# Kernel optimization log

Measured on AMD Instinct MI355X. Metric: run time of the kernel, lower is better.

The kernel has to match this reference:

```python
import jax, jax.numpy as jnp
import numpy as np

SIZES = [11793, 2948, 737, 184]   # vertices per mesh level, fine -> coarse
SPIRAL = [20, 14, 12, 9]          # spiral length per level
FILT = [128, 128, 64, 3]          # filters_dec[0]
LATENT = 128
BATCH = 16


def setup_inputs() -> dict:
    key = jax.random.key(0)
    ks = jax.random.split(key, 12)
    V = [s + 1 for s in SIZES]  # +1 dummy vertex per level
    inp = {}
    inp["z"] = jax.random.normal(ks[0], (BATCH, LATENT), jnp.float32)
    # dense upsampling matrices: level k+1 -> level k
    inp["U0"] = jax.random.normal(ks[1], (V[0], V[1]), jnp.float32) * 0.02
    inp["U1"] = jax.random.normal(ks[2], (V[1], V[2]), jnp.float32) * 0.02
    inp["U2"] = jax.random.normal(ks[3], (V[2], V[3]), jnp.float32) * 0.02
    # spiral index tables per level (shared across batch, values in [0, V))
    inp["S0"] = jax.random.randint(ks[4], (V[0], SPIRAL[0]), 0, V[0], dtype=jnp.int32)
    inp["S1"] = jax.random.randint(ks[5], (V[1], SPIRAL[1]), 0, V[1], dtype=jnp.int32)
    inp["S2"] = jax.random.randint(ks[6], (V[2], SPIRAL[2]), 0, V[2], dtype=jnp.int32)
    # fc_latent_dec: latent -> (sizes[-1]+1)*filters_dec[0][0]
    inp["Wfc"] = jax.random.normal(ks[7], (LATENT, V[3] * FILT[0]), jnp.float32) * 0.02
    inp["bfc"] = jnp.zeros((V[3] * FILT[0],), jnp.float32)
    # SpiralConv linear weights, stored (K*F_in, F_out), K-major flatten as in torch
    inp["W0"] = jax.random.normal(ks[8], (SPIRAL[2] * FILT[0], FILT[1]), jnp.float32) * 0.02
    inp["b0"] = jnp.zeros((FILT[1],), jnp.float32)
    inp["W1"] = jax.random.normal(ks[9], (SPIRAL[1] * FILT[1], FILT[2]), jnp.float32) * 0.02
    inp["b1"] = jnp.zeros((FILT[2],), jnp.float32)
    inp["W2"] = jax.random.normal(ks[10], (SPIRAL[0] * FILT[2], FILT[3]), jnp.float32) * 0.02
    inp["b2"] = jnp.zeros((FILT[3],), jnp.float32)
    return inp


def spiral_conv(x, S, W, b, elu):
    # x: (B, V, F); S: (V, K) vertex indices into the same level
    B, V, F = x.shape
    K = S.shape[1]
    g = jnp.take(x, S.reshape(-1), axis=1).reshape(B, V, K * F)  # gather, K-major flatten
    out = g @ W + b  # (B, V, F_out)
    if elu:
        out = jax.nn.elu(out)
    # zero out the dummy (last) vertex, as in Neural3DMM's zero_padding mask
    return out.at[:, -1, :].set(0.0)


def reference(z, U0, U1, U2, S0, S1, S2, Wfc, bfc, W0, b0, W1, b1, W2, b2):
    B = z.shape[0]
    x = (z @ Wfc + bfc).reshape(B, SIZES[-1] + 1, FILT[0])  # (B, 185, 128)
    x = jnp.einsum('vw,bwf->bvf', U2, x)                    # upsample -> (B, 738, 128)
    x = spiral_conv(x, S2, W0, b0, True)                    # (B, 738, 128)
    x = jnp.einsum('vw,bwf->bvf', U1, x)                    # (B, 2949, 128)
    x = spiral_conv(x, S1, W1, b1, True)                    # (B, 2949, 64)
    x = jnp.einsum('vw,bwf->bvf', U0, x)                    # (B, 11794, 64)
    x = spiral_conv(x, S0, W2, b2, False)                   # identity act -> (B, 11794, 3)
    return x
```

## Files before the change

### kernel.cpp

```cpp
#include <hip/hip_runtime.h>
#include <cmath>


#define NB 16

typedef __attribute__((ext_vector_type(8))) short bf16x8;
typedef __attribute__((ext_vector_type(4))) float f32x4;

__device__ __forceinline__ unsigned short f2bf(float x) {
    union { float f; unsigned u; } v; v.f = x;
    unsigned r = v.u + 0x7FFFu + ((v.u >> 16) & 1u);
    return (unsigned short)(r >> 16);
}
__device__ __forceinline__ void gload16(const void* src, void* dst) {
    __builtin_amdgcn_global_load_lds(
        (const __attribute__((address_space(1))) unsigned int*)src,
        (__attribute__((address_space(3))) unsigned int*)dst, 16, 0, 0);
}

__global__ __launch_bounds__(256) void cvt_u_all(
    const float* __restrict__ U0, const float* __restrict__ U1,
    const float* __restrict__ U2, unsigned short* __restrict__ Ub0,
    unsigned short* __restrict__ Ub1, unsigned short* __restrict__ Ub2) {
    int k = blockIdx.x * 256 + threadIdx.x;
    int r = blockIdx.y;
    const float* src;
    unsigned short* dst;
    int V, W, Wp, row;
    if (r < 11904) {
        src = U0; dst = Ub0; V = 11794; W = 2949; Wp = 2976; row = r;
    } else if (r < 11904 + 3072) {
        src = U1; dst = Ub1; V = 2949; W = 738; Wp = 768; row = r - 11904;
    } else {
        src = U2; dst = Ub2; V = 738; W = 185; Wp = 192; row = r - 11904 - 3072;
    }
    if (k >= Wp) return;
    float v = (row < V && k < W) ? src[(size_t)row * W + k] : 0.f;
    dst[(size_t)row * Wp + k] = f2bf(v);
}

__global__ __launch_bounds__(256) void cvt_misc(
    const float* __restrict__ W0, const float* __restrict__ W1,
    const float* __restrict__ W2, const int* __restrict__ S0,
    const int* __restrict__ S1, const int* __restrict__ S2,
    unsigned short* __restrict__ W0T, unsigned short* __restrict__ W1T,
    unsigned short* __restrict__ W2T, int* __restrict__ S0T,
    int* __restrict__ S1T, int* __restrict__ S2T) {
    const int N0 = 128 * 1536, N1 = 64 * 1792, N2 = 16 * 1288;
    const int N3 = 20 * 11794, N4 = 14 * 2949, N5 = 12 * 738;
    int id = blockIdx.x * 256 + threadIdx.x;
    if (id < N0) {
        int n = id / 1536, k = id - n * 1536;
        W0T[id] = f2bf(W0[(size_t)k * 128 + n]);
        return;
    }
    id -= N0;
    if (id < N1) {
        int n = id / 1792, k = id - n * 1792;
        W1T[id] = f2bf(W1[(size_t)k * 64 + n]);
        return;
    }
    id -= N1;
    if (id < N2) {
        int n = id / 1288, k = id - n * 1288;
        float v = (n < 3 && k < 1280) ? W2[(size_t)k * 3 + n] : 0.f;
        W2T[id] = f2bf(v);
        return;
    }
    id -= N2;
    if (id < N3) {
        int k = id / 11794, v = id - k * 11794;
        S0T[id] = S0[(size_t)v * 20 + k];
        return;
    }
    id -= N3;
    if (id < N4) {
        int k = id / 2949, v = id - k * 2949;
        S1T[id] = S1[(size_t)v * 14 + k];
        return;
    }
    id -= N4;
    if (id < N5) {
        int k = id / 738, v = id - k * 738;
        S2T[id] = S2[(size_t)v * 12 + k];
    }
}

__global__ __launch_bounds__(256) void fc_kernel(const float* __restrict__ z,
                                                 const float* __restrict__ Wfc,
                                                 const float* __restrict__ bfc,
                                                 unsigned short* __restrict__ x3T) {
    const int N = 185 * 128;
    __shared__ float zs[NB * 128];
    int t = threadIdx.x;
    for (int i = t; i < NB * 128; i += 256) zs[i] = z[i];
    __syncthreads();
    int n = blockIdx.x * 256 + t;
    if (n >= N) return;
    float acc[NB];
#pragma unroll
    for (int b = 0; b < NB; ++b) acc[b] = 0.f;
    for (int k = 0; k < 128; ++k) {
        float w = Wfc[k * N + n];
#pragma unroll
        for (int b = 0; b < NB; ++b) acc[b] = fmaf(zs[b * 128 + k], w, acc[b]);
    }
    float bv = bfc[n];
    int f = n & 127, v = n >> 7;
#pragma unroll
    for (int b = 0; b < NB; ++b)
        x3T[(size_t)(b * 128 + f) * 192 + v] = f2bf(acc[b] + bv);
    if (n < 7 * 128) {
        int vp = 185 + (n >> 7);
#pragma unroll
        for (int b = 0; b < NB; ++b)
            x3T[(size_t)(b * 128 + f) * 192 + vp] = 0;
    }
}

template<int FSH, int VP>
__global__ __launch_bounds__(256) void ups_mfma(
    const unsigned short* __restrict__ Ub, const unsigned short* __restrict__ xT,
    unsigned short* __restrict__ out,
    int WpA, int WpB, int nsteps, int gxsh, int q) {
    const int F = 1 << FSH;
    __shared__ __align__(16) unsigned short As[3][128 * 32];
    __shared__ __align__(16) unsigned short Bs[3][128 * 32];
    const int t = threadIdx.x;
    const int wv = t >> 6, lane = t & 63;
    const int lr = lane & 15;

    const int flat = blockIdx.x;
    const int wg = (flat & 7) * q + (flat >> 3);
    const int m0 = (wg >> gxsh) * 128;
    const int n0 = (wg & ((1 << gxsh) - 1)) * 128;

    const int srow = lane >> 2;
    const int schunk = (((lane & 3) - ((lane >> 3) & 3)) & 3) * 8;
    const int ii0 = wv * 2, ii1 = wv * 2 + 1;
    const unsigned short* asrc0 = Ub + (size_t)(m0 + ii0 * 16 + srow) * WpA + schunk;
    const unsigned short* asrc1 = Ub + (size_t)(m0 + ii1 * 16 + srow) * WpA + schunk;
    const unsigned short* bsrc0 = xT + (size_t)(n0 + ii0 * 16 + srow) * WpB + schunk;
    const unsigned short* bsrc1 = xT + (size_t)(n0 + ii1 * 16 + srow) * WpB + schunk;

    const int fslot = (((lane >> 4) + (lr >> 1)) & 3) * 8;
    const int wrow = (wv >> 1) * 64;
    const int wcol = (wv & 1) * 64;
    const int u0 = wv * 1024;

    f32x4 acc[4][4];
#pragma unroll
    for (int i = 0; i < 4; ++i)
#pragma unroll
        for (int j = 0; j < 4; ++j) acc[i][j] = {0.f, 0.f, 0.f, 0.f};

#define UPS_STAGE(off_, B_)                                             \
    {                                                                   \
        gload16(asrc0 + (off_), &As[B_][u0]);                           \
        gload16(bsrc0 + (off_), &Bs[B_][u0]);                           \
        gload16(asrc1 + (off_), &As[B_][u0 + 512]);                     \
        gload16(bsrc1 + (off_), &Bs[B_][u0 + 512]);                     \
    }
#define UPS_COMPUTE(B_)                                                 \
    {                                                                   \
        bf16x8 af[4], bg[4];                                            \
        _Pragma("unroll")                                               \
        for (int mt = 0; mt < 4; ++mt)                                  \
            af[mt] = *(const bf16x8*)&As[B_][(wrow + mt * 16 + lr) * 32 + fslot]; \
        _Pragma("unroll")                                               \
        for (int nt = 0; nt < 4; ++nt)                                  \
            bg[nt] = *(const bf16x8*)&Bs[B_][(wcol + nt * 16 + lr) * 32 + fslot]; \
        _Pragma("unroll")                                               \
        for (int mt = 0; mt < 4; ++mt)                                  \
            _Pragma("unroll")                                           \
            for (int nt = 0; nt < 4; ++nt)                              \
                acc[mt][nt] = __builtin_amdgcn_mfma_f32_16x16x32_bf16(  \
                    af[mt], bg[nt], acc[mt][nt], 0, 0, 0);              \
    }
#define UPS_WAIT4 asm volatile("s_waitcnt vmcnt(4)" ::: "memory"); __builtin_amdgcn_s_barrier();
#define UPS_WAIT0 asm volatile("s_waitcnt vmcnt(0)" ::: "memory"); __builtin_amdgcn_s_barrier();

    UPS_STAGE(0, 0);
    UPS_STAGE(32, 1);
    UPS_WAIT4;

    const int m = nsteps / 3;
    for (int it = 0; it < m - 1; ++it) {
        UPS_STAGE(64, 2);  UPS_COMPUTE(0); UPS_WAIT4;
        UPS_STAGE(96, 0);  UPS_COMPUTE(1); UPS_WAIT4;
        UPS_STAGE(128, 1); UPS_COMPUTE(2); UPS_WAIT4;
        asrc0 += 96; asrc1 += 96; bsrc0 += 96; bsrc1 += 96;
    }
    UPS_STAGE(64, 2);
    UPS_COMPUTE(0); UPS_WAIT4;
    UPS_COMPUTE(1); UPS_WAIT0;
    UPS_COMPUTE(2);
#undef UPS_STAGE
#undef UPS_COMPUTE
#undef UPS_WAIT4
#undef UPS_WAIT0

#pragma unroll
    for (int mt = 0; mt < 4; ++mt) {
        const int vb = m0 + wrow + mt * 16 + (lane >> 4) * 4;
#pragma unroll
        for (int nt = 0; nt < 4; ++nt) {
            const int col = n0 + wcol + nt * 16 + lr;
            const int b = col >> FSH, f = col & (F - 1);
            unsigned short* op = out + (size_t)b * VP * F + f;
#pragma unroll
            for (int j = 0; j < 4; ++j)
                op[(size_t)(vb + j) * F] = f2bf(acc[mt][nt][j]);
        }
    }
}

template<int VP>
__global__ __launch_bounds__(64) void conv_mfma(
    const unsigned short* __restrict__ xu, const int* __restrict__ ST,
    const unsigned short* __restrict__ WT, const float* __restrict__ bias,
    unsigned short* __restrict__ outT,
    int VT, int Ksp, int Kdim, int nsteps, int Fout) {
    __shared__ __align__(16) unsigned short As[2][32 * 32];
    __shared__ __align__(16) unsigned short Bs[2][64 * 32];
    const int lane = threadIdx.x;
    const int lr = lane & 15;
    const int m0 = blockIdx.x * 32;
    const int n0 = blockIdx.y * 64;
    const int b = m0 / VP;
    const int v0 = m0 - b * VP;
    const unsigned short* xb = xu + (((size_t)b * VP) << 7);

    const int arow = lane >> 1;
    const int h = lane & 1;
    const int vg = (v0 + arow < VT) ? (v0 + arow) : (VT - 1);
    const int schunk = (((lane & 3) - ((lane >> 3) & 3)) & 3) * 8;
    const int fslot = (((lane >> 4) + (lr >> 1)) & 3) * 8;
    int sw0 = arow * 32 + (((2 * h + 0 + ((lane >> 2) & 3)) & 3) * 8);
    int sw1 = arow * 32 + (((2 * h + 1 + ((lane >> 2) & 3)) & 3) * 8);

    int s_c = 0;
    int idx_c = ST[vg];
    int idx_n = ST[(size_t)VT + vg];

    f32x4 acc[2][4];
#pragma unroll
    for (int i = 0; i < 2; ++i)
#pragma unroll
        for (int j = 0; j < 4; ++j) acc[i][j] = {0.f, 0.f, 0.f, 0.f};

#define CONV_COMPUTE(B_)                                                \
    {                                                                   \
        bf16x8 af[2], bg[4];                                            \
        _Pragma("unroll")                                               \
        for (int mt = 0; mt < 2; ++mt)                                  \
            af[mt] = *(const bf16x8*)&As[B_][(mt * 16 + lr) * 32 + fslot]; \
        _Pragma("unroll")                                               \
        for (int nt = 0; nt < 4; ++nt)                                  \
            bg[nt] = *(const bf16x8*)&Bs[B_][(nt * 16 + lr) * 32 + fslot]; \
        _Pragma("unroll")                                               \
        for (int mt = 0; mt < 2; ++mt)                                  \
            _Pragma("unroll")                                           \
            for (int nt = 0; nt < 4; ++nt)                              \
                acc[mt][nt] = __builtin_amdgcn_mfma_f32_16x16x32_bf16(  \
                    af[mt], bg[nt], acc[mt][nt], 0, 0, 0);              \
    }
#define CONV_BODY(tn_, CUR_, NXT_)                                      \
    {                                                                   \
        const int k0 = (tn_) * 32;                                      \
        const int sn = k0 >> 7;                                         \
        const int idx = (sn != s_c) ? idx_n : idx_c;                    \
        const unsigned short* p = xb + (((size_t)idx) << 7) + (k0 & 127) + h * 16; \
        bf16x8 g0 = *(const bf16x8*)(p);                                \
        bf16x8 g1 = *(const bf16x8*)(p + 8);                            \
        _Pragma("unroll")                                               \
        for (int i = 0; i < 4; ++i) {                                   \
            const int n = n0 + i * 16 + (lane >> 2);                    \
            gload16(WT + (size_t)n * Kdim + k0 + schunk, &Bs[NXT_][i * 512]); \
        }                                                               \
        if (sn != s_c) {                                                \
            idx_c = idx_n; s_c = sn;                                    \
            if (s_c + 1 < Ksp) idx_n = ST[(size_t)(s_c + 1) * VT + vg]; \
        }                                                               \
        CONV_COMPUTE(CUR_);                                             \
        *(bf16x8*)&As[NXT_][sw0] = g0;                                  \
        *(bf16x8*)&As[NXT_][sw1] = g1;                                  \
        __syncthreads();                                                \
    }

    {
        const unsigned short* p = xb + (((size_t)idx_c) << 7) + h * 16;
        bf16x8 g0 = *(const bf16x8*)(p);
        bf16x8 g1 = *(const bf16x8*)(p + 8);
#pragma unroll
        for (int i = 0; i < 4; ++i) {
            const int n = n0 + i * 16 + (lane >> 2);
            gload16(WT + (size_t)n * Kdim + schunk, &Bs[0][i * 512]);
        }
        *(bf16x8*)&As[0][sw0] = g0;
        *(bf16x8*)&As[0][sw1] = g1;
    }
    __syncthreads();

    for (int ts = 0; ts + 2 < nsteps; ts += 2) {
        CONV_BODY(ts + 1, 0, 1);
        CONV_BODY(ts + 2, 1, 0);
    }
    CONV_BODY(nsteps - 1, 0, 1);
    CONV_COMPUTE(1);
#undef CONV_BODY
#undef CONV_COMPUTE

#pragma unroll
    for (int nt = 0; nt < 4; ++nt) {
        const int n = n0 + nt * 16 + lr;
        const float bv = bias[n];
        unsigned short* op = outT + (size_t)(b * Fout + n) * VP;
#pragma unroll
        for (int mt = 0; mt < 2; ++mt) {
            const int v = v0 + mt * 16 + (lane >> 4) * 4;
            ushort4 stv;
#pragma unroll
            for (int j = 0; j < 4; ++j) {
                float val = acc[mt][nt][j] + bv;
                val = val > 0.f ? val : expm1f(val);
                if (v + j == VT - 1) val = 0.f;
                ((unsigned short*)&stv)[j] = f2bf(val);
            }
            *(ushort4*)(op + v) = stv;
        }
    }
}

__global__ __launch_bounds__(64) void out_mfma(
    const unsigned short* __restrict__ xu, const int* __restrict__ ST,
    const unsigned short* __restrict__ W2T, const float* __restrict__ b2,
    float* __restrict__ out) {
    const int VT = 11794, VP = 11904, TPB = 372;
    __shared__ __align__(16) unsigned short As[2][32 * 32];
    const int lane = threadIdx.x;
    const int lr = lane & 15;
    const int lko = (lane >> 4) * 8;
    const int bm = blockIdx.x;
    const int b = bm / TPB;
    const int v0 = (bm - b * TPB) * 32;
    const unsigned short* xb = xu + ((size_t)b * VP << 6);

    const int arow = lane >> 1;
    const int h = lane & 1;
    const int v = v0 + arow;
    const int vg = v < VT ? v : VT - 1;
    int sw0 = arow * 32 + (((2 * h + 0 + ((lane >> 2) & 3)) & 3) * 8);
    int sw1 = arow * 32 + (((2 * h + 1 + ((lane >> 2) & 3)) & 3) * 8);
    const int fslot = (((lane >> 4) + (lr >> 1)) & 3) * 8;

    int s_c = 0;
    int idx_c = ST[vg];
    int idx_n = ST[VT + vg];

    f32x4 acc[2];
    acc[0] = {0.f, 0.f, 0.f, 0.f};
    acc[1] = {0.f, 0.f, 0.f, 0.f};

    const unsigned short* wrow = W2T + (size_t)lr * 1288 + lko;
    bf16x8 bg_c = *(const bf16x8*)(wrow);

#define OUT_COMPUTE(B_)                                                 \
    {                                                                   \
        bf16x8 af[2];                                                   \
        _Pragma("unroll")                                               \
        for (int mt = 0; mt < 2; ++mt)                                  \
            af[mt] = *(const bf16x8*)&As[B_][(mt * 16 + lr) * 32 + fslot]; \
        _Pragma("unroll")                                               \
        for (int mt = 0; mt < 2; ++mt)                                  \
            acc[mt] = __builtin_amdgcn_mfma_f32_16x16x32_bf16(af[mt], bg_c, acc[mt], 0, 0, 0); \
    }
#define OUT_BODY(tn_, CUR_, NXT_)                                       \
    {                                                                   \
        const int k0 = (tn_) * 32;                                      \
        const int sn = k0 >> 6;                                         \
        const int idx = (sn != s_c) ? idx_n : idx_c;                    \
        const unsigned short* p = xb + (((size_t)idx) << 6) + (k0 & 63) + h * 16; \
        bf16x8 g0 = *(const bf16x8*)(p);                                \
        bf16x8 g1 = *(const bf16x8*)(p + 8);                            \
        bf16x8 bg_n = *(const bf16x8*)(wrow + k0);                      \
        if (sn != s_c) {                                                \
            idx_c = idx_n; s_c = sn;                                    \
            if (s_c + 1 < 20) idx_n = ST[(size_t)(s_c + 1) * VT + vg];  \
        }                                                               \
        OUT_COMPUTE(CUR_);                                              \
        bg_c = bg_n;                                                    \
        *(bf16x8*)&As[NXT_][sw0] = g0;                                  \
        *(bf16x8*)&As[NXT_][sw1] = g1;                                  \
        __syncthreads();                                                \
    }

    {
        const unsigned short* p = xb + ((size_t)idx_c << 6) + h * 16;
        bf16x8 g0 = *(const bf16x8*)(p);
        bf16x8 g1 = *(const bf16x8*)(p + 8);
        *(bf16x8*)&As[0][sw0] = g0;
        *(bf16x8*)&As[0][sw1] = g1;
    }
    __syncthreads();

    const int nsteps = 40;
    for (int ts = 0; ts + 2 < nsteps; ts += 2) {
        OUT_BODY(ts + 1, 0, 1);
        OUT_BODY(ts + 2, 1, 0);
    }
    OUT_BODY(nsteps - 1, 0, 1);
    OUT_COMPUTE(1);
#undef OUT_BODY
#undef OUT_COMPUTE

    if (lr < 3) {
        const float bv = b2[lr];
#pragma unroll
        for (int mt = 0; mt < 2; ++mt) {
#pragma unroll
            for (int j = 0; j < 4; ++j) {
                const int vv = v0 + mt * 16 + (lane >> 4) * 4 + j;
                if (vv < VT) {
                    float val = acc[mt][j] + bv;
                    if (vv == VT - 1) val = 0.f;
                    out[((size_t)b * VT + vv) * 3 + lr] = val;
                }
            }
        }
    }
}

extern "C" void kernel_launch(void* const* d_in, const int* in_sizes, int n_in,
                              void* d_out, int out_size, void* d_ws, size_t ws_size,
                              hipStream_t stream) {
    const float* z   = (const float*)d_in[0];
    const float* U0  = (const float*)d_in[1];
    const float* U1  = (const float*)d_in[2];
    const float* U2  = (const float*)d_in[3];
    const int*   S0  = (const int*)d_in[4];
    const int*   S1  = (const int*)d_in[5];
    const int*   S2  = (const int*)d_in[6];
    const float* Wfc = (const float*)d_in[7];
    const float* bfc = (const float*)d_in[8];
    const float* W0  = (const float*)d_in[9];
    const float* b0  = (const float*)d_in[10];
    const float* W1  = (const float*)d_in[11];
    const float* b1  = (const float*)d_in[12];
    const float* W2  = (const float*)d_in[13];
    const float* b2  = (const float*)d_in[14];
    float* out = (float*)d_out;

    char* ws = (char*)d_ws;
    unsigned short* Ub0 = (unsigned short*)(ws + 0);
    unsigned short* Ub1 = (unsigned short*)(ws + 70852608);
    unsigned short* Ub2 = (unsigned short*)(ws + 75571200);
    unsigned short* x3T = (unsigned short*)(ws + 75866112);
    unsigned short* x2u = (unsigned short*)(ws + 76652544);
    unsigned short* x2T = (unsigned short*)(ws + 79798272);
    unsigned short* x1u = (unsigned short*)(ws + 82944000);
    unsigned short* x1T = (unsigned short*)(ws + 95526912);
    unsigned short* x0u = (unsigned short*)(ws + 101818368);
    unsigned short* W0T = (unsigned short*)(ws + 126197760);
    unsigned short* W1T = (unsigned short*)(ws + 126590976);
    int* S1T = (int*)(ws + 126820352);
    int* S2T = (int*)(ws + 126985504);
    int* S0T = (int*)(ws + 127020928);
    unsigned short* W2T = (unsigned short*)(ws + 127964448);

    cvt_u_all<<<dim3(12, 11904 + 3072 + 768), 256, 0, stream>>>(U0, U1, U2, Ub0, Ub1, Ub2);
    {
        const int total = 128 * 1536 + 64 * 1792 + 16 * 1288 +
                          20 * 11794 + 14 * 2949 + 12 * 738;
        cvt_misc<<<dim3((total + 255) / 256), 256, 0, stream>>>(
            W0, W1, W2, S0, S1, S2, W0T, W1T, W2T, S0T, S1T, S2T);
    }

    fc_kernel<<<dim3((185 * 128 + 255) / 256), 256, 0, stream>>>(z, Wfc, bfc, x3T);
    ups_mfma<7, 768><<<dim3(96), 256, 0, stream>>>(Ub2, x3T, x2u, 192, 192, 6, 4, 12);
    conv_mfma<768><<<dim3(384, 2), 64, 0, stream>>>(x2u, S2T, W0T, b0, x2T, 738, 12, 1536, 48, 128);
    ups_mfma<7, 3072><<<dim3(384), 256, 0, stream>>>(Ub1, x2T, x1u, 768, 768, 24, 4, 48);
    conv_mfma<3072><<<dim3(1536, 1), 64, 0, stream>>>(x1u, S1T, W1T, b1, x1T, 2949, 14, 1792, 56, 64);
    ups_mfma<6, 11904><<<dim3(744), 256, 0, stream>>>(Ub0, x1T, x0u, 2976, 3072, 93, 3, 93);
    out_mfma<<<dim3(16 * 372), 64, 0, stream>>>(x0u, S0T, W2T, b2, out);
}
```

Measured before the change: 362.9 us.

## Fully unroll spiral conv loops, preload indices, drop barriers for waitcnt pipelining

conv_mfma now takes the step count and spiral length as template parameters. Both conv_mfma and out_mfma load every spiral index into registers up front and fully unroll the K loop. conv_mfma triple-buffers the weight tiles in LDS and replaces __syncthreads with explicit s_waitcnt vmcnt so more global loads stay in flight. out_mfma drops its barriers, relying on single-wave in-order LDS access. This removes per-step branch, index-fetch and barrier overhead, at the cost of more registers and reliance on correct manual wait counts.

```diff
diff --git a/kernel.cpp b/kernel.cpp
--- a/kernel.cpp
+++ b/kernel.cpp
@@ -215,14 +215,14 @@
     }
 }
 
-template<int VP>
+template<int VP, int NSTEPS, int KSP>
 __global__ __launch_bounds__(64) void conv_mfma(
     const unsigned short* __restrict__ xu, const int* __restrict__ ST,
     const unsigned short* __restrict__ WT, const float* __restrict__ bias,
     unsigned short* __restrict__ outT,
-    int VT, int Ksp, int Kdim, int nsteps, int Fout) {
+    int VT, int Kdim, int Fout) {
     __shared__ __align__(16) unsigned short As[2][32 * 32];
-    __shared__ __align__(16) unsigned short Bs[2][64 * 32];
+    __shared__ __align__(16) unsigned short Bs[3][64 * 32];
     const int lane = threadIdx.x;
     const int lr = lane & 15;
     const int m0 = blockIdx.x * 32;
@@ -236,12 +236,12 @@
     const int vg = (v0 + arow < VT) ? (v0 + arow) : (VT - 1);
     const int schunk = (((lane & 3) - ((lane >> 3) & 3)) & 3) * 8;
     const int fslot = (((lane >> 4) + (lr >> 1)) & 3) * 8;
-    int sw0 = arow * 32 + (((2 * h + 0 + ((lane >> 2) & 3)) & 3) * 8);
-    int sw1 = arow * 32 + (((2 * h + 1 + ((lane >> 2) & 3)) & 3) * 8);
-
-    int s_c = 0;
-    int idx_c = ST[vg];
-    int idx_n = ST[(size_t)VT + vg];
+    const int sw0 = arow * 32 + (((2 * h + 0 + ((lane >> 2) & 3)) & 3) * 8);
+    const int sw1 = arow * 32 + (((2 * h + 1 + ((lane >> 2) & 3)) & 3) * 8);
+
+    int idx[KSP];
+#pragma unroll
+    for (int k = 0; k < KSP; ++k) idx[k] = ST[(size_t)k * VT + vg];
 
     f32x4 acc[2][4];
 #pragma unroll
@@ -249,15 +249,17 @@
 #pragma unroll
         for (int j = 0; j < 4; ++j) acc[i][j] = {0.f, 0.f, 0.f, 0.f};
 
-#define CONV_COMPUTE(B_)                                                \
+    bf16x8 gA[2][2];
+
+#define CC(AB_, BB_)                                                    \
     {                                                                   \
         bf16x8 af[2], bg[4];                                            \
         _Pragma("unroll")                                               \
         for (int mt = 0; mt < 2; ++mt)                                  \
-            af[mt] = *(const bf16x8*)&As[B_][(mt * 16 + lr) * 32 + fslot]; \
+            af[mt] = *(const bf16x8*)&As[AB_][(mt * 16 + lr) * 32 + fslot]; \
         _Pragma("unroll")                                               \
         for (int nt = 0; nt < 4; ++nt)                                  \
-            bg[nt] = *(const bf16x8*)&Bs[B_][(nt * 16 + lr) * 32 + fslot]; \
+            bg[nt] = *(const bf16x8*)&Bs[BB_][(nt * 16 + lr) * 32 + fslot]; \
         _Pragma("unroll")                                               \
         for (int mt = 0; mt < 2; ++mt)                                  \
             _Pragma("unroll")                                           \
@@ -265,51 +267,61 @@
                 acc[mt][nt] = __builtin_amdgcn_mfma_f32_16x16x32_bf16(  \
                     af[mt], bg[nt], acc[mt][nt], 0, 0, 0);              \
     }
-#define CONV_BODY(tn_, CUR_, NXT_)                                      \
-    {                                                                   \
-        const int k0 = (tn_) * 32;                                      \
-        const int sn = k0 >> 7;                                         \
-        const int idx = (sn != s_c) ? idx_n : idx_c;                    \
-        const unsigned short* p = xb + (((size_t)idx) << 7) + (k0 & 127) + h * 16; \
-        bf16x8 g0 = *(const bf16x8*)(p);                                \
-        bf16x8 g1 = *(const bf16x8*)(p + 8);                            \
-        _Pragma("unroll")                                               \
-        for (int i = 0; i < 4; ++i) {                                   \
-            const int n = n0 + i * 16 + (lane >> 2);                    \
-            gload16(WT + (size_t)n * Kdim + k0 + schunk, &Bs[NXT_][i * 512]); \
-        }                                                               \
-        if (sn != s_c) {                                                \
-            idx_c = idx_n; s_c = sn;                                    \
-            if (s_c + 1 < Ksp) idx_n = ST[(size_t)(s_c + 1) * VT + vg]; \
-        }                                                               \
-        CONV_COMPUTE(CUR_);                                             \
-        *(bf16x8*)&As[NXT_][sw0] = g0;                                  \
-        *(bf16x8*)&As[NXT_][sw1] = g1;                                  \
-        __syncthreads();                                                \
-    }
 
     {
-        const unsigned short* p = xb + (((size_t)idx_c) << 7) + h * 16;
-        bf16x8 g0 = *(const bf16x8*)(p);
-        bf16x8 g1 = *(const bf16x8*)(p + 8);
+        const unsigned short* p = xb + (((size_t)idx[0]) << 7) + h * 16;
+        gA[0][0] = *(const bf16x8*)(p);
+        gA[0][1] = *(const bf16x8*)(p + 8);
 #pragma unroll
         for (int i = 0; i < 4; ++i) {
             const int n = n0 + i * 16 + (lane >> 2);
             gload16(WT + (size_t)n * Kdim + schunk, &Bs[0][i * 512]);
         }
-        *(bf16x8*)&As[0][sw0] = g0;
-        *(bf16x8*)&As[0][sw1] = g1;
-    }
-    __syncthreads();
-
-    for (int ts = 0; ts + 2 < nsteps; ts += 2) {
-        CONV_BODY(ts + 1, 0, 1);
-        CONV_BODY(ts + 2, 1, 0);
-    }
-    CONV_BODY(nsteps - 1, 0, 1);
-    CONV_COMPUTE(1);
-#undef CONV_BODY
-#undef CONV_COMPUTE
+#pragma unroll
+        for (int i = 0; i < 4; ++i) {
+            const int n = n0 + i * 16 + (lane >> 2);
+            gload16(WT + (size_t)n * Kdim + 32 + schunk, &Bs[1][i * 512]);
+        }
+        *(bf16x8*)&As[0][sw0] = gA[0][0];
+        *(bf16x8*)&As[0][sw1] = gA[0][1];
+        asm volatile("s_waitcnt vmcnt(4)" ::: "memory");
+    }
+
+#pragma unroll
+    for (int ts = 0; ts < NSTEPS - 2; ++ts) {
+        const int tn1 = ts + 1, tn2 = ts + 2;
+        {
+            const unsigned short* p =
+                xb + (((size_t)idx[tn1 >> 2]) << 7) + (tn1 & 3) * 32 + h * 16;
+            gA[tn1 & 1][0] = *(const bf16x8*)(p);
+            gA[tn1 & 1][1] = *(const bf16x8*)(p + 8);
+        }
+        {
+            const int k0 = tn2 * 32;
+#pragma unroll
+            for (int i = 0; i < 4; ++i) {
+                const int n = n0 + i * 16 + (lane >> 2);
+                gload16(WT + (size_t)n * Kdim + k0 + schunk, &Bs[tn2 % 3][i * 512]);
+            }
+        }
+        CC(ts & 1, ts % 3);
+        asm volatile("s_waitcnt vmcnt(4)" ::: "memory");
+        *(bf16x8*)&As[tn1 & 1][sw0] = gA[tn1 & 1][0];
+        *(bf16x8*)&As[tn1 & 1][sw1] = gA[tn1 & 1][1];
+    }
+    {
+        const int tn1 = NSTEPS - 1;
+        const unsigned short* p =
+            xb + (((size_t)idx[tn1 >> 2]) << 7) + (tn1 & 3) * 32 + h * 16;
+        gA[tn1 & 1][0] = *(const bf16x8*)(p);
+        gA[tn1 & 1][1] = *(const bf16x8*)(p + 8);
+        CC((NSTEPS - 2) & 1, (NSTEPS - 2) % 3);
+        asm volatile("s_waitcnt vmcnt(0)" ::: "memory");
+        *(bf16x8*)&As[tn1 & 1][sw0] = gA[tn1 & 1][0];
+        *(bf16x8*)&As[tn1 & 1][sw1] = gA[tn1 & 1][1];
+    }
+    CC((NSTEPS - 1) & 1, (NSTEPS - 1) % 3);
+#undef CC
 
 #pragma unroll
     for (int nt = 0; nt < 4; ++nt) {
@@ -336,7 +348,7 @@
     const unsigned short* __restrict__ xu, const int* __restrict__ ST,
     const unsigned short* __restrict__ W2T, const float* __restrict__ b2,
     float* __restrict__ out) {
-    const int VT = 11794, VP = 11904, TPB = 372;
+    const int VT = 11794, VP = 11904, TPB = 372, NSTEPS = 40;
     __shared__ __align__(16) unsigned short As[2][32 * 32];
     const int lane = threadIdx.x;
     const int lr = lane & 15;
@@ -350,69 +362,56 @@
     const int h = lane & 1;
     const int v = v0 + arow;
     const int vg = v < VT ? v : VT - 1;
-    int sw0 = arow * 32 + (((2 * h + 0 + ((lane >> 2) & 3)) & 3) * 8);
-    int sw1 = arow * 32 + (((2 * h + 1 + ((lane >> 2) & 3)) & 3) * 8);
+    const int sw0 = arow * 32 + (((2 * h + 0 + ((lane >> 2) & 3)) & 3) * 8);
+    const int sw1 = arow * 32 + (((2 * h + 1 + ((lane >> 2) & 3)) & 3) * 8);
     const int fslot = (((lane >> 4) + (lr >> 1)) & 3) * 8;
 
-    int s_c = 0;
-    int idx_c = ST[vg];
-    int idx_n = ST[VT + vg];
+    int idx[20];
+#pragma unroll
+    for (int k = 0; k < 20; ++k) idx[k] = ST[(size_t)k * VT + vg];
 
     f32x4 acc[2];
     acc[0] = {0.f, 0.f, 0.f, 0.f};
     acc[1] = {0.f, 0.f, 0.f, 0.f};
 
     const unsigned short* wrow = W2T + (size_t)lr * 1288 + lko;
-    bf16x8 bg_c = *(const bf16x8*)(wrow);
-
-#define OUT_COMPUTE(B_)                                                 \
+    bf16x8 gA[2][2], bgr[2];
+
+#define OC(AB_, WB_)                                                    \
     {                                                                   \
         bf16x8 af[2];                                                   \
         _Pragma("unroll")                                               \
         for (int mt = 0; mt < 2; ++mt)                                  \
-            af[mt] = *(const bf16x8*)&As[B_][(mt * 16 + lr) * 32 + fslot]; \
+            af[mt] = *(const bf16x8*)&As[AB_][(mt * 16 + lr) * 32 + fslot]; \
         _Pragma("unroll")                                               \
         for (int mt = 0; mt < 2; ++mt)                                  \
-            acc[mt] = __builtin_amdgcn_mfma_f32_16x16x32_bf16(af[mt], bg_c, acc[mt], 0, 0, 0); \
-    }
-#define OUT_BODY(tn_, CUR_, NXT_)                                       \
-    {                                                                   \
-        const int k0 = (tn_) * 32;                                      \
-        const int sn = k0 >> 6;                                         \
-        const int idx = (sn != s_c) ? idx_n : idx_c;                    \
-        const unsigned short* p = xb + (((size_t)idx) << 6) + (k0 & 63) + h * 16; \
-        bf16x8 g0 = *(const bf16x8*)(p);                                \
-        bf16x8 g1 = *(const bf16x8*)(p + 8);                            \
-        bf16x8 bg_n = *(const bf16x8*)(wrow + k0);                      \
-        if (sn != s_c) {                                                \
-            idx_c = idx_n; s_c = sn;                                    \
-            if (s_c + 1 < 20) idx_n = ST[(size_t)(s_c + 1) * VT + vg];  \
-        }                                                               \
-        OUT_COMPUTE(CUR_);                                              \
-        bg_c = bg_n;                                                    \
-        *(bf16x8*)&As[NXT_][sw0] = g0;                                  \
-        *(bf16x8*)&As[NXT_][sw1] = g1;                                  \
-        __syncthreads();                                                \
+            acc[mt] = __builtin_amdgcn_mfma_f32_16x16x32_bf16(          \
+                af[mt], bgr[WB_], acc[mt], 0, 0, 0);                    \
     }
 
     {
-        const unsigned short* p = xb + ((size_t)idx_c << 6) + h * 16;
-        bf16x8 g0 = *(const bf16x8*)(p);
-        bf16x8 g1 = *(const bf16x8*)(p + 8);
-        *(bf16x8*)&As[0][sw0] = g0;
-        *(bf16x8*)&As[0][sw1] = g1;
-    }
-    __syncthreads();
-
-    const int nsteps = 40;
-    for (int ts = 0; ts + 2 < nsteps; ts += 2) {
-        OUT_BODY(ts + 1, 0, 1);
-        OUT_BODY(ts + 2, 1, 0);
-    }
-    OUT_BODY(nsteps - 1, 0, 1);
-    OUT_COMPUTE(1);
-#undef OUT_BODY
-#undef OUT_COMPUTE
+        const unsigned short* p = xb + (((size_t)idx[0]) << 6) + h * 16;
+        gA[0][0] = *(const bf16x8*)(p);
+        gA[0][1] = *(const bf16x8*)(p + 8);
+        bgr[0] = *(const bf16x8*)(wrow);
+        *(bf16x8*)&As[0][sw0] = gA[0][0];
+        *(bf16x8*)&As[0][sw1] = gA[0][1];
+    }
+
+#pragma unroll
+    for (int ts = 0; ts < NSTEPS - 1; ++ts) {
+        const int tn = ts + 1;
+        const unsigned short* p =
+            xb + (((size_t)idx[tn >> 1]) << 6) + (tn & 1) * 32 + h * 16;
+        gA[tn & 1][0] = *(const bf16x8*)(p);
+        gA[tn & 1][1] = *(const bf16x8*)(p + 8);
+        bgr[tn & 1] = *(const bf16x8*)(wrow + tn * 32);
+        OC(ts & 1, ts & 1);
+        *(bf16x8*)&As[tn & 1][sw0] = gA[tn & 1][0];
+        *(bf16x8*)&As[tn & 1][sw1] = gA[tn & 1][1];
+    }
+    OC((NSTEPS - 1) & 1, (NSTEPS - 1) & 1);
+#undef OC
 
     if (lr < 3) {
         const float bv = b2[lr];
@@ -478,9 +477,11 @@
 
     fc_kernel<<<dim3((185 * 128 + 255) / 256), 256, 0, stream>>>(z, Wfc, bfc, x3T);
     ups_mfma<7, 768><<<dim3(96), 256, 0, stream>>>(Ub2, x3T, x2u, 192, 192, 6, 4, 12);
-    conv_mfma<768><<<dim3(384, 2), 64, 0, stream>>>(x2u, S2T, W0T, b0, x2T, 738, 12, 1536, 48, 128);
+    conv_mfma<768, 48, 12><<<dim3(384, 2), 64, 0, stream>>>(
+        x2u, S2T, W0T, b0, x2T, 738, 1536, 128);
     ups_mfma<7, 3072><<<dim3(384), 256, 0, stream>>>(Ub1, x2T, x1u, 768, 768, 24, 4, 48);
-    conv_mfma<3072><<<dim3(1536, 1), 64, 0, stream>>>(x1u, S1T, W1T, b1, x1T, 2949, 14, 1792, 56, 64);
+    conv_mfma<3072, 56, 14><<<dim3(1536, 1), 64, 0, stream>>>(
+        x1u, S1T, W1T, b1, x1T, 2949, 1792, 64);
     ups_mfma<6, 11904><<<dim3(744), 256, 0, stream>>>(Ub0, x1T, x0u, 2976, 3072, 93, 3, 93);
     out_mfma<<<dim3(16 * 372), 64, 0, stream>>>(x0u, S0T, W2T, b2, out);
 }
```

New measurement: 353.6 us. 1.03x faster.
